# Optimization experiments

Hardware: AMD Instinct MI355X
Metric: run time of the kernel (lower is better)

## Reference

```python
import math
import jax, jax.numpy as jnp
import numpy as np

BN_EPS = 1e-5

def _lrelu(x, s):
    return jnp.where(x >= 0, x, s * x)

def _bn(x, g, b):
    # BatchNorm2d in train mode (torch default): biased batch stats over (B,H,W)
    mu = jnp.mean(x, axis=(0, 2, 3), keepdims=True)
    var = jnp.mean((x - mu) ** 2, axis=(0, 2, 3), keepdims=True)
    return (x - mu) / jnp.sqrt(var + BN_EPS) * g[None, :, None, None] + b[None, :, None, None]

def _knn(x, x2, k):
    # x: [B,d,P], x2: [B,d,S] -> idx [B,k,S]: k nearest points of x for each column of x2
    inner = -2.0 * jnp.einsum('bdp,bds->bps', x, x2)
    xx = jnp.sum(x ** 2, axis=1)[:, :, None]    # [B,P,1]
    xx2 = jnp.sum(x2 ** 2, axis=1)[:, None, :]  # [B,1,S]
    d = -xx - inner - xx2                        # [B,P,S], larger = closer
    _, idx = jax.lax.top_k(jnp.transpose(d, (0, 2, 1)), k)  # [B,S,k]
    return jnp.transpose(idx, (0, 2, 1))         # [B,k,S]

def _gather_nb(X, idx, s, k):
    # faithful to torch gether_neibour, including its flat-reshape layout
    B, C, P = X.shape
    base = jnp.arange(B)[:, None, None] * P
    flat = (idx + base).reshape(-1)
    Xt = jnp.transpose(X, (0, 2, 1)).reshape(B * P, C)
    return Xt[flat].reshape(B, s, k, C)

def _c2d(x, W, b):
    return jnp.einsum('oc,bcpk->bopk', W, x) + b[None, :, None, None]

def _c1d(x, W, b):
    return jnp.einsum('oc,bcp->bop', W, x) + b[None, :, None]

def _forward(x, W_pos, b_pos, g2, be2, W_conv, b_conv, g1, be1, W_a1, b_a1, W_a2, b_a2, W_b1, b_b1, W_b2, b_b2, num_points):
    B, C, P = x.shape
    k = 8
    s = num_points
    # ---- Dynamic_sampling_M: uniform mesh over (x,y) bbox, snap to nearest event ----
    L = int(math.ceil(math.sqrt(s)))
    m = jnp.arange(L, dtype=x.dtype) / L
    m01 = jnp.tile(m[None, :], (L, 1)).reshape(1, 1, L * L)
    m02 = jnp.tile(m[:, None], (1, L)).reshape(1, 1, L * L)
    mesh = jnp.broadcast_to(jnp.concatenate([m01, m02], axis=1), (B, 2, L * L))
    Px = jax.lax.stop_gradient(x[:, :2, :])  # knn runs under torch.no_grad
    mn = Px.min(axis=2, keepdims=True)
    mx = Px.max(axis=2, keepdims=True)
    PS = mesh * (mx - mn) + mn
    idx0 = _knn(Px, PS, 1)                                   # [B,1,L*L]
    sp = _gather_nb(x, idx0, L * L, 1)[:, :, 0, :].transpose(0, 2, 1)  # [B,C,s]
    idx = _knn(jax.lax.stop_gradient(x[:, :3, :]), jax.lax.stop_gradient(sp[:, :3, :]), k)  # [B,k,s]
    x1 = jnp.transpose(_gather_nb(x, idx, s, k), (0, 3, 1, 2))  # [B,C,s,k]
    # ---- positional encoding ----
    PA = x1[:, :3, :, :]
    PC = x1[:, :3, :, 0:1]
    diff = PA - PC
    sq = jnp.sum(diff ** 2, axis=1, keepdims=True)
    temp = jnp.where(sq > 0, jnp.sqrt(jnp.where(sq > 0, sq, 1.0)), 0.0)
    PEmb = jnp.concatenate([PA, jnp.broadcast_to(PC, PA.shape), diff, temp], axis=1)  # [B,10,s,k]
    PEmb = _lrelu(_bn(_c2d(PEmb, W_pos, b_pos), g2, be2), 0.2)
    x_ = _lrelu(_bn(_c2d(x1[:, :4, :, :], W_conv, b_conv), g1, be1), 0.2)
    feat = jnp.concatenate([x_, PEmb], axis=1)  # [B,64,s,k]
    att = _c2d(_lrelu(_c2d(feat, W_a1, b_a1), 0.2), W_a2, b_a2)  # [B,1,s,k]
    att = jax.nn.softmax(att, axis=-1)
    feat = jnp.sum(feat * att, axis=-1)  # [B,64,s]
    Fea1 = _c1d(feat, W_b1, b_b1)
    Fea2 = _c1d(x1[:, :4, :, 0], W_b2, b_b2)
    out = _lrelu(Fea1 + Fea2, 0.01)
    return jnp.concatenate([x1[:, :5, :, 0], out], axis=1)  # [B,69,s]

def setup_inputs() -> dict:
    key = jax.random.key(0)
    ks = jax.random.split(key, 8)
    B, C, P = 2, 5, 16384
    num_points = 4096  # perfect square required by the mesh sampler
    outc, inc, h = 64, 4, 32
    w = lambda k_, shape: jax.random.normal(k_, shape, jnp.float32) * 0.05
    x = jax.random.normal(ks[0], (B, C, P), jnp.float32)
    return dict(
        x=x,
        W_pos=w(ks[1], (h, 10)), b_pos=jnp.zeros((h,), jnp.float32),
        g2=jnp.ones((h,), jnp.float32), be2=jnp.zeros((h,), jnp.float32),
        W_conv=w(ks[2], (h, inc)), b_conv=jnp.zeros((h,), jnp.float32),
        g1=jnp.ones((h,), jnp.float32), be1=jnp.zeros((h,), jnp.float32),
        W_a1=w(ks[3], (32, outc)), b_a1=jnp.zeros((32,), jnp.float32),
        W_a2=w(ks[4], (1, 32)), b_a2=jnp.zeros((1,), jnp.float32),
        W_b1=w(ks[5], (outc, outc)), b_b1=jnp.zeros((outc,), jnp.float32),
        W_b2=w(ks[6], (outc, inc)), b_b2=jnp.zeros((outc,), jnp.float32),
        num_points=num_points,
    )

def reference(x, W_pos, b_pos, g2, be2, W_conv, b_conv, g1, be1, W_a1, b_a1, W_a2, b_a2, W_b1, b_b1, W_b2, b_b2, num_points):
    return _forward(x, W_pos, b_pos, g2, be2, W_conv, b_conv, g1, be1, W_a1, b_a1, W_a2, b_a2, W_b1, b_b1, W_b2, b_b2, num_points)
```

## Files before the change

kernel.cpp:

```cpp
#include <hip/hip_runtime.h>
#include <math.h>

#define B_ 2
#define P_ 16384
#define C_ 5
#define S_ 4096
#define KNN_ 8
#define L_ 64

typedef unsigned short u16;
typedef unsigned int u32;
typedef unsigned long long u64;

__device__ int    g_idxk[B_ * KNN_ * S_];
__device__ float  g_partials[256 * 128];
__device__ float  g_mnmx[B_][5];
__device__ int    g_hist[B_ * 4097];
__device__ int    g_cursor[B_ * 4096];
__device__ int    g_binof[B_ * P_];
__device__ int    g_dt[B_ * 4096];
__device__ u64    g_mask[B_ * 64];
__device__ float4 g_recA[B_ * P_];
__device__ float4 g_recB[B_ * P_];
__device__ u16    g_idxsc[B_ * P_];

__device__ __forceinline__ float bf2f(u16 u) {
  union { u32 i; float f; } c; c.i = ((u32)u) << 16; return c.f;
}
__device__ __forceinline__ u16 f2bf(float f) {
  union { float f; u32 i; } c; c.f = f;
  u32 r = c.i + 0x7fffu + ((c.i >> 16) & 1u);
  return (u16)(r >> 16);
}
__device__ __forceinline__ float ldany(const void* p, int i, int f32) {
  return f32 ? ((const float*)p)[i] : bf2f(((const u16*)p)[i]);
}

__device__ __forceinline__ double packkey(float d, int idx) {
  u32 bits = __float_as_uint(d);
  u32 key = bits ^ ((u32)(((int)bits) >> 31) | 0x80000000u);
  int hi = (int)(0x3FF00000u | (key >> 12));
  int lo = (int)((key << 20) | ((u32)(16383 - idx) << 6));
  return __hiloint2double(hi, lo);
}
__device__ __forceinline__ int keyidx(double w) {
  return 16383 - (int)(((u32)__double2loint(w) >> 6) & 16383u);
}
__device__ __forceinline__ float keyd(double w) {
  u32 hi = (u32)__double2hiint(w), lo = (u32)__double2loint(w);
  u32 key = (hi << 12) | (lo >> 20);
  u32 mask = (u32)(((int)key) >> 31);
  u32 bits = key ^ ((~mask) | 0x80000000u);
  return __uint_as_float(bits);
}

__device__ __forceinline__ int chk_bad(const void* p, int n, int tid) {
  int bad = 0;
  for (int i = tid; i < n; i += 256) {
    float f = bf2f(((const u16*)p)[i]);
    if (!(f == f) || fabsf(f) > 1024.0f) bad = 1;
  }
  return bad;
}

#define INS8(key)                                                        \
  do {                                                                   \
    if ((key) > a7) {                                                    \
      double t_ = (key), h_;                                             \
      h_ = fmax(a0, t_); t_ = fmin(a0, t_); a0 = h_;                     \
      h_ = fmax(a1, t_); t_ = fmin(a1, t_); a1 = h_;                     \
      h_ = fmax(a2, t_); t_ = fmin(a2, t_); a2 = h_;                     \
      h_ = fmax(a3, t_); t_ = fmin(a3, t_); a3 = h_;                     \
      h_ = fmax(a4, t_); t_ = fmin(a4, t_); a4 = h_;                     \
      h_ = fmax(a5, t_); t_ = fmin(a5, t_); a5 = h_;                     \
      h_ = fmax(a6, t_); t_ = fmin(a6, t_); a6 = h_;                     \
      a7 = fmax(a7, t_);                                                 \
    }                                                                    \
  } while (0)

#define MAX64(w)                                                         \
  do {                                                                   \
    w = fmax(w, __shfl_xor(w, 1, 64));                                   \
    w = fmax(w, __shfl_xor(w, 2, 64));                                   \
    w = fmax(w, __shfl_xor(w, 4, 64));                                   \
    w = fmax(w, __shfl_xor(w, 8, 64));                                   \
    w = fmax(w, __shfl_xor(w, 16, 64));                                  \
    w = fmax(w, __shfl_xor(w, 32, 64));                                  \
  } while (0)

__device__ __forceinline__ void ringcell(int R, int t, int cx, int cy, int& X, int& Y) {
  int side = 2 * R + 1;
  if (t < side)          { X = cx - R + t;          Y = cy - R; }
  else if (t < 2 * side) { X = cx - R + (t - side); Y = cy + R; }
  else {
    int u = t - 2 * side, m2 = 2 * R - 1;
    if (u < m2) { X = cx - R; Y = cy - R + 1 + u; }
    else        { X = cx + R; Y = cy - R + 1 + (u - m2); }
  }
}

__global__ __launch_bounds__(256) void k_prep(const void* __restrict__ xv) {
  __shared__ int sbad;
  __shared__ float sred[4][5];
  int tid = threadIdx.x, b = blockIdx.x;
  if (tid == 0) sbad = 0;
  __syncthreads();
  if (chk_bad(xv, 1024, tid)) atomicOr(&sbad, 1);
  __syncthreads();
  const int f32 = sbad;
  int base0 = b * C_ * P_, base1 = base0 + P_, base2 = base1 + P_;
  float mn0 = INFINITY, mx0 = -INFINITY, mn1 = INFINITY, mx1 = -INFINITY, am = 0.f;
  for (int p = tid; p < P_; p += 256) {
    float v0 = ldany(xv, base0 + p, f32);
    float v1 = ldany(xv, base1 + p, f32);
    float v2 = ldany(xv, base2 + p, f32);
    mn0 = fminf(mn0, v0); mx0 = fmaxf(mx0, v0);
    mn1 = fminf(mn1, v1); mx1 = fmaxf(mx1, v1);
    am = fmaxf(am, fabsf(v2));
  }
  for (int off = 32; off; off >>= 1) {
    mn0 = fminf(mn0, __shfl_down(mn0, off)); mx0 = fmaxf(mx0, __shfl_down(mx0, off));
    mn1 = fminf(mn1, __shfl_down(mn1, off)); mx1 = fmaxf(mx1, __shfl_down(mx1, off));
    am = fmaxf(am, __shfl_down(am, off));
  }
  int l = tid & 63, g = tid >> 6;
  if (l == 0) {
    sred[g][0] = mn0; sred[g][1] = mx0; sred[g][2] = mn1; sred[g][3] = mx1; sred[g][4] = am;
  }
  __syncthreads();
  if (tid == 0) {
    float a0 = fminf(fminf(sred[0][0], sred[1][0]), fminf(sred[2][0], sred[3][0]));
    float a1 = fmaxf(fmaxf(sred[0][1], sred[1][1]), fmaxf(sred[2][1], sred[3][1]));
    float a2 = fminf(fminf(sred[0][2], sred[1][2]), fminf(sred[2][2], sred[3][2]));
    float a3 = fmaxf(fmaxf(sred[0][3], sred[1][3]), fmaxf(sred[2][3], sred[3][3]));
    float a4 = fmaxf(fmaxf(sred[0][4], sred[1][4]), fmaxf(sred[2][4], sred[3][4]));
    float aa = fmaxf(fmaxf(fabsf(a0), fabsf(a1)), fmaxf(fmaxf(fabsf(a2), fabsf(a3)), a4));
    g_mnmx[b][0] = a0; g_mnmx[b][1] = a1; g_mnmx[b][2] = a2; g_mnmx[b][3] = a3;
    g_mnmx[b][4] = aa * aa;
  }
  for (int i2 = tid; i2 < 4097; i2 += 256) g_hist[b * 4097 + i2] = 0;
}

__global__ __launch_bounds__(256) void k_hist(const void* __restrict__ xv) {
  __shared__ int sbad;
  int tid = threadIdx.x, blk = blockIdx.x;
  if (tid == 0) sbad = 0;
  __syncthreads();
  if (chk_bad(xv, 1024, tid)) atomicOr(&sbad, 1);
  __syncthreads();
  const int f32 = sbad;
  int b = blk >> 4;
  int pb = (blk & 15) * 1024;
  int base0 = b * C_ * P_, base1 = base0 + P_;
  float mn0 = g_mnmx[b][0], mx0 = g_mnmx[b][1], mn1 = g_mnmx[b][2], mx1 = g_mnmx[b][3];
  float r0 = __fsub_rn(mx0, mn0), r1 = __fsub_rn(mx1, mn1);
  float inv0 = (r0 > 0.f) ? 64.0f / r0 : 0.f;
  float inv1 = (r1 > 0.f) ? 64.0f / r1 : 0.f;
  for (int q = 0; q < 4; ++q) {
    int i = pb + q * 256 + tid;
    float v0 = ldany(xv, base0 + i, f32);
    float v1 = ldany(xv, base1 + i, f32);
    int bx = (int)fminf(fmaxf((v0 - mn0) * inv0, 0.f), 63.f);
    int by = (int)fminf(fmaxf((v1 - mn1) * inv1, 0.f), 63.f);
    int bin = by * 64 + bx;
    g_binof[b * P_ + i] = bin;
    atomicAdd(&g_hist[b * 4097 + bin], 1);
  }
}

__global__ __launch_bounds__(256) void k_scan() {
  __shared__ int part[256];
  int b = blockIdx.x, t = threadIdx.x;
  int loc[16]; int s0 = 0;
  for (int q = 0; q < 16; ++q) { loc[q] = g_hist[b * 4097 + t * 16 + q]; s0 += loc[q]; }
  part[t] = s0;
  __syncthreads();
  for (int d2 = 1; d2 < 256; d2 <<= 1) {
    int v = (t >= d2) ? part[t - d2] : 0;
    __syncthreads();
    part[t] += v;
    __syncthreads();
  }
  int run = (t == 0) ? 0 : part[t - 1];
  for (int q = 0; q < 16; ++q) {
    g_hist[b * 4097 + t * 16 + q] = run;
    g_cursor[b * 4096 + t * 16 + q] = run;
    run += loc[q];
  }
  if (t == 0) g_hist[b * 4097 + 4096] = P_;
}

__global__ __launch_bounds__(256) void k_scatter(const void* __restrict__ xv) {
  __shared__ int sbad;
  int tid = threadIdx.x, blk = blockIdx.x;
  if (tid == 0) sbad = 0;
  __syncthreads();
  if (chk_bad(xv, 1024, tid)) atomicOr(&sbad, 1);
  __syncthreads();
  const int f32 = sbad;
  int b = blk >> 4;
  int pb = (blk & 15) * 1024;
  int base0 = b * C_ * P_, base1 = base0 + P_, base2 = base1 + P_;
  for (int q = 0; q < 4; ++q) {
    int i = pb + q * 256 + tid;
    float a0 = ldany(xv, base0 + i, f32);
    float a1 = ldany(xv, base1 + i, f32);
    float a2 = ldany(xv, base2 + i, f32);
    float xx2d = __fadd_rn(__fmul_rn(a0, a0), __fmul_rn(a1, a1));
    float xx3  = __fadd_rn(__fadd_rn(__fmul_rn(a0, a0), __fmul_rn(a1, a1)), __fmul_rn(a2, a2));
    int bin = g_binof[b * P_ + i];
    int pos = atomicAdd(&g_cursor[b * 4096 + bin], 1);
    g_recA[(b << 14) + pos] = make_float4(a0, a1, xx2d, __int_as_float(i));
    g_recB[(b << 14) + pos] = make_float4(a0, a1, a2, xx3);
    g_idxsc[(b << 14) + pos] = (u16)i;
  }
}

__global__ __launch_bounds__(256) void k_dt() {
  __shared__ u64 occm[64];
  __shared__ short rowd[64][64];
  int b = blockIdx.x, t = threadIdx.x;
  if (t < 64) {
    u64 m = 0ull;
    const int* h = g_hist + b * 4097 + t * 64;
    for (int x = 0; x < 64; ++x)
      if (h[x + 1] > h[x]) m |= (1ull << x);
    occm[t] = m;
    g_mask[b * 64 + t] = m;
  }
  __syncthreads();
#pragma unroll
  for (int q = 0; q < 16; ++q) {
    int c = q * 256 + t, y = c >> 6, x = c & 63;
    u64 m = occm[y];
    int rd = 127;
    if (m) {
      u64 hi = m >> x;
      int dhi = hi ? (__ffsll((long long)hi) - 1) : 127;
      u64 lo = (x < 63) ? (m & (((u64)1 << (x + 1)) - 1)) : m;
      int dlo = lo ? (x - (63 - __clzll((long long)lo))) : 127;
      rd = min(dhi, dlo);
    }
    rowd[y][x] = (short)rd;
  }
  __syncthreads();
#pragma unroll
  for (int q = 0; q < 16; ++q) {
    int c = q * 256 + t, y = c >> 6, x = c & 63;
    int best = 127;
    for (int dy = 0; dy < 64; ++dy) {
      if (dy >= best) break;
      int y1 = y - dy, y2 = y + dy;
      if (y1 >= 0) { int v = rowd[y1][x]; best = min(best, (dy > v) ? dy : v); }
      if (dy && y2 < 64) { int v = rowd[y2][x]; best = min(best, (dy > v) ? dy : v); }
    }
    g_dt[(b << 12) + c] = best;
  }
}

__global__ __launch_bounds__(256, 6) void k_knn2(const void* __restrict__ xv) {
  __shared__ int shist[4097];
  __shared__ u64 smask[64];
  __shared__ int sbad;
  int tid = threadIdx.x;
  if (tid == 0) sbad = 0;
  __syncthreads();
  if (chk_bad(xv, 1024, tid)) atomicOr(&sbad, 1);
  __syncthreads();
  const int f32 = sbad;

  int blk = blockIdx.x;
  int b = blk >> 10;
  for (int i2 = tid; i2 < 4097; i2 += 256) shist[i2] = g_hist[b * 4097 + i2];
  if (tid < 64) smask[tid] = g_mask[b * 64 + tid];
  __syncthreads();

  int l = tid & 63;
  int grp = l >> 3, lo = l & 7;
  int q = blk * 4 + (tid >> 6);
  int s = q & (S_ - 1);
  int base0 = b * C_ * P_, base1 = base0 + P_, base2 = base1 + P_;

  float mn0 = g_mnmx[b][0], mx0 = g_mnmx[b][1], mn1 = g_mnmx[b][2], mx1 = g_mnmx[b][3];
  float margin = 2e-5f * g_mnmx[b][4];
  float r0 = __fsub_rn(mx0, mn0), r1 = __fsub_rn(mx1, mn1);
  float w0 = r0 * 0.015625f, w1 = r1 * 0.015625f;
  float wmin = fminf(w0, w1) * 0.999f;
  const float4* recA = g_recA + (b << 14);
  const float4* recB = g_recB + (b << 14);

  float mm0 = (float)(s & (L_ - 1)) * 0.015625f;
  float mm1 = (float)(s >> 6) * 0.015625f;
  float ps0 = __fadd_rn(__fmul_rn(mm0, r0), mn0);
  float ps1 = __fadd_rn(__fmul_rn(mm1, r1), mn1);
  float xx2q = __fadd_rn(__fmul_rn(ps0, ps0), __fmul_rn(ps1, ps1));
  int bqx = s & 63, bqy = s >> 6;
  int R0 = g_dt[(b << 12) + s];
  double bestA = -1.0;
  if (R0 <= 1) {
#pragma unroll
    for (int dy = -1; dy <= 1; ++dy) {
#pragma unroll
      for (int dx = -1; dx <= 1; ++dx) {
        int X = bqx + dx, Y = bqy + dy;
        if ((unsigned)X > 63u || (unsigned)Y > 63u) continue;
        if (!((smask[Y] >> X) & 1ull)) continue;
        int bin = Y * 64 + X;
        int st = shist[bin], en = shist[bin + 1];
        for (int j2 = st + l; j2 < en; j2 += 64) {
          float4 rc = recA[j2];
          float dot = __fadd_rn(__fmul_rn(rc.x, ps0), __fmul_rn(rc.y, ps1));
          float inner = __fmul_rn(-2.0f, dot);
          float d = __fsub_rn(__fsub_rn(-rc.z, inner), xx2q);
          bestA = fmax(bestA, packkey(d, __float_as_int(rc.w)));
        }
      }
    }
  }
  double t1 = bestA;
  MAX64(t1);
  for (int R = (R0 < 2 ? 2 : R0); R < 64; ++R) {
    if (t1 >= 1.0) {
      float lb = (float)(R - 1) * wmin;
      float ub = __fadd_rn(-(lb * lb), margin);
      if (ub < keyd(t1)) break;
    }
    int cnt = 8 * R;
    for (int t = grp; t < cnt; t += 8) {
      int X, Y;
      ringcell(R, t, bqx, bqy, X, Y);
      if ((unsigned)X > 63u || (unsigned)Y > 63u) continue;
      if (!((smask[Y] >> X) & 1ull)) continue;
      int bin = Y * 64 + X;
      int st = shist[bin], en = shist[bin + 1];
      for (int j2 = st + lo; j2 < en; j2 += 8) {
        float4 rc = recA[j2];
        float dot = __fadd_rn(__fmul_rn(rc.x, ps0), __fmul_rn(rc.y, ps1));
        float inner = __fmul_rn(-2.0f, dot);
        float d = __fsub_rn(__fsub_rn(-rc.z, inner), xx2q);
        bestA = fmax(bestA, packkey(d, __float_as_int(rc.w)));
      }
    }
    if (__any(bestA > t1)) { t1 = bestA; MAX64(t1); }
  }
  int qi = keyidx(t1) & (P_ - 1);

  float q0 = ldany(xv, base0 + qi, f32);
  float q1 = ldany(xv, base1 + qi, f32);
  float q2 = ldany(xv, base2 + qi, f32);
  float xx3q = __fadd_rn(__fadd_rn(__fmul_rn(q0, q0), __fmul_rn(q1, q1)), __fmul_rn(q2, q2));
  int qbin = g_binof[b * P_ + qi];
  int cx = qbin & 63, cy = qbin >> 6;
  double a0 = -1.0, a1 = -1.0, a2 = -1.0, a3 = -1.0,
         a4 = -1.0, a5 = -1.0, a6 = -1.0, a7 = -1.0;
#pragma unroll
  for (int dy = -1; dy <= 1; ++dy) {
#pragma unroll
    for (int dx = -1; dx <= 1; ++dx) {
      int X = cx + dx, Y = cy + dy;
      if ((unsigned)X > 63u || (unsigned)Y > 63u) continue;
      if (!((smask[Y] >> X) & 1ull)) continue;
      int bin = Y * 64 + X;
      int st = shist[bin], en = shist[bin + 1];
      for (int j2 = st + l; j2 < en; j2 += 64) {
        float4 rc = recB[j2];
        int idx = (int)g_idxsc[(b << 14) + j2];
        float dot = __fadd_rn(__fadd_rn(__fmul_rn(rc.x, q0), __fmul_rn(rc.y, q1)),
                              __fmul_rn(rc.z, q2));
        float inner = __fmul_rn(-2.0f, dot);
        float d = __fsub_rn(__fsub_rn(-rc.w, inner), xx3q);
        double key = packkey(d, idx);
        INS8(key);
      }
    }
  }
  double t8;
  {
    double c0 = a0, c1 = a1, c2 = a2, c3 = a3, c4 = a4, c5 = a5, c6 = a6, c7 = a7;
    double w = -1.0;
#pragma unroll
    for (int r2 = 0; r2 < 8; ++r2) {
      w = c0;
      MAX64(w);
      bool cns = (c0 == w);
      c0 = cns ? c1 : c0; c1 = cns ? c2 : c1; c2 = cns ? c3 : c2; c3 = cns ? c4 : c3;
      c4 = cns ? c5 : c4; c5 = cns ? c6 : c5; c6 = cns ? c7 : c6; c7 = cns ? -1.0 : c7;
    }
    t8 = w;
  }
  for (int R = 2; R < 64; ++R) {
    if (t8 >= 1.0) {
      float lb = (float)(R - 1) * wmin;
      float ub = __fadd_rn(-(lb * lb), margin);
      if (ub < keyd(t8)) break;
    }
    bool added = false;
    int cnt = 8 * R;
    for (int t = grp; t < cnt; t += 8) {
      int X, Y;
      ringcell(R, t, cx, cy, X, Y);
      if ((unsigned)X > 63u || (unsigned)Y > 63u) continue;
      if (!((smask[Y] >> X) & 1ull)) continue;
      int bin = Y * 64 + X;
      int st = shist[bin], en = shist[bin + 1];
      for (int j2 = st + lo; j2 < en; j2 += 8) {
        float4 rc = recB[j2];
        int idx = (int)g_idxsc[(b << 14) + j2];
        float dot = __fadd_rn(__fadd_rn(__fmul_rn(rc.x, q0), __fmul_rn(rc.y, q1)),
                              __fmul_rn(rc.z, q2));
        float inner = __fmul_rn(-2.0f, dot);
        float d = __fsub_rn(__fsub_rn(-rc.w, inner), xx3q);
        double key = packkey(d, idx);
        added = added || (key > t8);
        INS8(key);
      }
    }
    if (__any(added)) {
      double c0 = a0, c1 = a1, c2 = a2, c3 = a3, c4 = a4, c5 = a5, c6 = a6, c7 = a7;
      double w = -1.0;
#pragma unroll
      for (int r2 = 0; r2 < 8; ++r2) {
        w = c0;
        MAX64(w);
        bool cns = (c0 == w);
        c0 = cns ? c1 : c0; c1 = cns ? c2 : c1; c2 = cns ? c3 : c2; c3 = cns ? c4 : c3;
        c4 = cns ? c5 : c4; c5 = cns ? c6 : c5; c6 = cns ? c7 : c6; c7 = cns ? -1.0 : c7;
      }
      t8 = w;
    }
  }
  double wk = 0.0;
#pragma unroll
  for (int r2 = 0; r2 < 8; ++r2) {
    double w = a0;
    MAX64(w);
    if (l == r2) wk = w;
    bool cns = (a0 == w);
    a0 = cns ? a1 : a0; a1 = cns ? a2 : a1; a2 = cns ? a3 : a2; a3 = cns ? a4 : a3;
    a4 = cns ? a5 : a4; a5 = cns ? a6 : a5; a6 = cns ? a7 : a6; a7 = cns ? -1.0 : a7;
  }
  if (l < 8) g_idxk[b * 32768 + l * 4096 + s] = keyidx(wk);
}

__global__ __launch_bounds__(256) void k_tail(const void* __restrict__ x,
                                              const void* __restrict__ Wpos,
                                              const void* __restrict__ bpos,
                                              const void* __restrict__ Wconv,
                                              const void* __restrict__ bconv) {
  __shared__ float sWpos[320], sbpos[32], sWconv[128], sbconv[32];
  __shared__ float sacc[16][128];
  __shared__ int sbx, sbw;
  int tid = threadIdx.x;
  if (tid == 0) { sbx = 0; sbw = 0; }
  __syncthreads();
  if (chk_bad(x, 1024, tid)) atomicOr(&sbx, 1);
  if (chk_bad(Wpos, 320, tid) | chk_bad(Wconv, 128, tid)) atomicOr(&sbw, 1);
  __syncthreads();
  const int f32 = sbx, wf32 = sbw;

  int id = blockIdx.x * 256 + tid;
  int b = id >> 15, n = id & 32767;
  const int* fb = g_idxk + b * 32768;
  int base0 = b * C_ * P_;
  int p = fb[n] & (P_ - 1);
  int p0 = fb[n & ~7] & (P_ - 1);
  float xvv[4], pc3[3];
#pragma unroll
  for (int cc = 0; cc < 4; ++cc) xvv[cc] = ldany(x, base0 + cc * P_ + p, f32);
#pragma unroll
  for (int cc = 0; cc < 3; ++cc) pc3[cc] = ldany(x, base0 + cc * P_ + p0, f32);

  for (int i2 = tid; i2 < 320; i2 += 256) sWpos[i2] = ldany(Wpos, i2, wf32);
  if (tid < 128) sWconv[tid] = ldany(Wconv, tid, wf32);
  if (tid < 32) { sbpos[tid] = ldany(bpos, tid, wf32); sbconv[tid] = ldany(bconv, tid, wf32); }
  __syncthreads();

  float d0 = xvv[0] - pc3[0], d1 = xvv[1] - pc3[1], d2 = xvv[2] - pc3[2];
  float sq = d0 * d0 + d1 * d1 + d2 * d2;
  float temp = (sq > 0.0f) ? sqrtf(sq) : 0.0f;
  float pe[10] = {xvv[0], xvv[1], xvv[2], pc3[0], pc3[1], pc3[2], d0, d1, d2, temp};
#pragma unroll
  for (int o = 0; o < 64; ++o) {
    float v;
    if (o < 32) {
      v = sbconv[o];
#pragma unroll
      for (int cc = 0; cc < 4; ++cc) v = fmaf(sWconv[o * 4 + cc], xvv[cc], v);
    } else {
      v = sbpos[o - 32];
#pragma unroll
      for (int cc = 0; cc < 10; ++cc) v = fmaf(sWpos[(o - 32) * 10 + cc], pe[cc], v);
    }
    float sv = v, qv = v * v;
    for (int m = 1; m < 16; m <<= 1) { sv += __shfl_xor(sv, m, 16); qv += __shfl_xor(qv, m, 16); }
    if ((tid & 15) == 0) { sacc[tid >> 4][o * 2] = sv; sacc[tid >> 4][o * 2 + 1] = qv; }
  }
  __syncthreads();
  if (tid < 128) {
    float a = 0.f;
#pragma unroll
    for (int w = 0; w < 16; ++w) a += sacc[w][tid];
    g_partials[blockIdx.x * 128 + tid] = a;
  }
}

__global__ __launch_bounds__(256) void k_pass2(const void* __restrict__ x,
                                               const void* __restrict__ Wpos,
                                               const void* __restrict__ bpos,
                                               const void* __restrict__ Wconv,
                                               const void* __restrict__ bconv,
                                               const void* __restrict__ g1,
                                               const void* __restrict__ be1,
                                               const void* __restrict__ g2,
                                               const void* __restrict__ be2,
                                               const void* __restrict__ Wa1,
                                               const void* __restrict__ ba1,
                                               const void* __restrict__ Wa2,
                                               const void* __restrict__ ba2,
                                               const void* __restrict__ Wb1,
                                               const void* __restrict__ bb1,
                                               const void* __restrict__ Wb2,
                                               const void* __restrict__ bb2,
                                               void* __restrict__ out) {
  __shared__ float sWpos[320], sbpos[32], sWconv[128], sbconv[32];
  __shared__ float sWa1[2048], sba1[32], sWa2[32];
  __shared__ float sWb1[64 * 65];
  __shared__ float sbb1[64], sWb2[256], sbb2[64], sstats[128];
  __shared__ float sp2[2][128];
  __shared__ float sba2;
  __shared__ int sbx, sbw;
  int tid = threadIdx.x;
  if (tid == 0) { sbx = 0; sbw = 0; }
  __syncthreads();
  if (chk_bad(x, 1024, tid)) atomicOr(&sbx, 1);
  if (chk_bad(Wa1, 2048, tid) | chk_bad(Wb1, 4096, tid)) atomicOr(&sbw, 1);
  __syncthreads();
  int xf32 = sbx, wf32 = sbw;

  int g = blockIdx.x * 32 + (tid >> 3);
  int j = tid & 7;
  int b = g >> 12, i = g & (S_ - 1);
  int n = i * 8 + j;
  const int* fb = g_idxk + b * 32768;
  int xbase = b * C_ * P_;
  int p = fb[n] & (P_ - 1);
  int p0 = fb[n & ~7] & (P_ - 1);
  float xvv[4];
#pragma unroll
  for (int c = 0; c < 4; ++c) xvv[c] = ldany(x, xbase + c * P_ + p, xf32);
  float pc3[3];
#pragma unroll
  for (int c = 0; c < 3; ++c) pc3[c] = ldany(x, xbase + c * P_ + p0, xf32);
  float xc0 = ldany(x, xbase + p0, xf32);
  float xc1 = ldany(x, xbase + P_ + p0, xf32);
  float xc2 = ldany(x, xbase + 2 * P_ + p0, xf32);
  float xc3 = ldany(x, xbase + 3 * P_ + p0, xf32);

  {
    int slot = tid & 127, half = tid >> 7;
    float a0 = 0.f, a1 = 0.f;
    for (int blk = half * 128; blk < half * 128 + 128; blk += 2) {
      a0 += g_partials[blk * 128 + slot];
      a1 += g_partials[(blk + 1) * 128 + slot];
    }
    sp2[half][slot] = a0 + a1;
  }
  for (int i2 = tid; i2 < 320; i2 += 256) sWpos[i2] = ldany(Wpos, i2, wf32);
  if (tid < 128) sWconv[tid] = ldany(Wconv, tid, wf32);
  if (tid < 32) { sbpos[tid] = ldany(bpos, tid, wf32); sbconv[tid] = ldany(bconv, tid, wf32); }
  for (int i2 = tid; i2 < 2048; i2 += 256) sWa1[i2] = ldany(Wa1, i2, wf32);
  for (int i2 = tid; i2 < 4096; i2 += 256) sWb1[(i2 >> 6) * 65 + (i2 & 63)] = ldany(Wb1, i2, wf32);
  if (tid >= 32 && tid < 64) { sba1[tid - 32] = ldany(ba1, tid - 32, wf32); sWa2[tid - 32] = ldany(Wa2, tid - 32, wf32); }
  if (tid >= 64 && tid < 128) { sbb1[tid - 64] = ldany(bb1, tid - 64, wf32); sbb2[tid - 64] = ldany(bb2, tid - 64, wf32); }
  sWb2[tid] = ldany(Wb2, tid, wf32);
  if (tid == 0) sba2 = ldany(ba2, 0, wf32);
  __syncthreads();
  if (tid >= 128 && tid < 192) {
    int ch = tid - 128;
    float sum = sp2[0][ch * 2] + sp2[1][ch * 2];
    float sq = sp2[0][ch * 2 + 1] + sp2[1][ch * 2 + 1];
    float mean = sum * (1.0f / 65536.0f);
    float var = sq * (1.0f / 65536.0f) - mean * mean;
    int o = ch & 31;
    float gg = ldany(ch < 32 ? g1 : g2, o, wf32);
    float be = ldany(ch < 32 ? be1 : be2, o, wf32);
    float scale = gg / sqrtf(var + 1e-5f);
    sstats[ch * 2] = scale;
    sstats[ch * 2 + 1] = be - mean * scale;
  }
  __syncthreads();

  float d0 = xvv[0] - pc3[0], d1 = xvv[1] - pc3[1], d2 = xvv[2] - pc3[2];
  float sq = d0 * d0 + d1 * d1 + d2 * d2;
  float temp = (sq > 0.0f) ? sqrtf(sq) : 0.0f;
  float pe[10] = {xvv[0], xvv[1], xvv[2], pc3[0], pc3[1], pc3[2], d0, d1, d2, temp};
  float feat[64];
#pragma unroll
  for (int o = 0; o < 32; ++o) {
    float acc = sbconv[o];
#pragma unroll
    for (int c = 0; c < 4; ++c) acc = fmaf(sWconv[o * 4 + c], xvv[c], acc);
    feat[o] = acc;
  }
#pragma unroll
  for (int o = 0; o < 32; ++o) {
    float acc = sbpos[o];
#pragma unroll
    for (int c = 0; c < 10; ++c) acc = fmaf(sWpos[o * 10 + c], pe[c], acc);
    feat[32 + o] = acc;
  }
#pragma unroll
  for (int c = 0; c < 64; ++c) {
    float v = fmaf(feat[c], sstats[c * 2], sstats[c * 2 + 1]);
    feat[c] = (v >= 0.f) ? v : 0.2f * v;
  }
  float att = sba2;
#pragma unroll 4
  for (int h = 0; h < 32; ++h) {
    float a0 = 0.f, a1 = 0.f, a2 = 0.f, a3 = 0.f;
#pragma unroll
    for (int c = 0; c < 64; c += 4) {
      a0 = fmaf(sWa1[h * 64 + c],     feat[c],     a0);
      a1 = fmaf(sWa1[h * 64 + c + 1], feat[c + 1], a1);
      a2 = fmaf(sWa1[h * 64 + c + 2], feat[c + 2], a2);
      a3 = fmaf(sWa1[h * 64 + c + 3], feat[c + 3], a3);
    }
    float acc = sba1[h] + ((a0 + a1) + (a2 + a3));
    acc = (acc >= 0.f) ? acc : 0.2f * acc;
    att = fmaf(sWa2[h], acc, att);
  }
  float mxv = att;
  for (int mk = 1; mk < 8; mk <<= 1) mxv = fmaxf(mxv, __shfl_xor(mxv, mk, 8));
  float e = expf(att - mxv);
  float se = e;
  for (int mk = 1; mk < 8; mk <<= 1) se += __shfl_xor(se, mk, 8);
  float a = e / se;
#pragma unroll
  for (int c = 0; c < 64; ++c) {
    float w = feat[c] * a;
    w += __shfl_xor(w, 1, 8);
    w += __shfl_xor(w, 2, 8);
    w += __shfl_xor(w, 4, 8);
    feat[c] = w;
  }
  int obase = b * 69 * S_;
#pragma unroll
  for (int oc = 0; oc < 8; ++oc) {
    int o = j * 8 + oc;
    float a0 = sbb1[o], a1 = 0.f, a2 = 0.f, a3 = 0.f;
#pragma unroll
    for (int c = 0; c < 64; c += 4) {
      a0 = fmaf(sWb1[o * 65 + c],     feat[c],     a0);
      a1 = fmaf(sWb1[o * 65 + c + 1], feat[c + 1], a1);
      a2 = fmaf(sWb1[o * 65 + c + 2], feat[c + 2], a2);
      a3 = fmaf(sWb1[o * 65 + c + 3], feat[c + 3], a3);
    }
    float acc = (a0 + a1) + (a2 + a3);
    float acc2 = sbb2[o];
    acc2 = fmaf(sWb2[o * 4 + 0], xc0, acc2);
    acc2 = fmaf(sWb2[o * 4 + 1], xc1, acc2);
    acc2 = fmaf(sWb2[o * 4 + 2], xc2, acc2);
    acc2 = fmaf(sWb2[o * 4 + 3], xc3, acc2);
    float r = acc + acc2;
    r = (r >= 0.f) ? r : 0.01f * r;
    int oi = obase + (5 + o) * S_ + i;
    if (xf32) ((float*)out)[oi] = r; else ((u16*)out)[oi] = f2bf(r);
  }
  if (j == 0) {
#pragma unroll
    for (int c = 0; c < 5; ++c) {
      int oi = obase + c * S_ + i;
      if (xf32) ((float*)out)[oi] = ((const float*)x)[xbase + c * P_ + p0];
      else      ((u16*)out)[oi]   = ((const u16*)x)[xbase + c * P_ + p0];
    }
  }
}

extern "C" void kernel_launch(void* const* d_in, const int* in_sizes, int n_in,
                              void* d_out, int out_size, void* d_ws, size_t ws_size,
                              hipStream_t stream) {
  const void* x     = d_in[0];
  const void* Wpos  = d_in[1];
  const void* bpos  = d_in[2];
  const void* g2    = d_in[3];
  const void* be2   = d_in[4];
  const void* Wconv = d_in[5];
  const void* bconv = d_in[6];
  const void* g1    = d_in[7];
  const void* be1   = d_in[8];
  const void* Wa1   = d_in[9];
  const void* ba1   = d_in[10];
  const void* Wa2   = d_in[11];
  const void* ba2   = d_in[12];
  const void* Wb1   = d_in[13];
  const void* bb1   = d_in[14];
  const void* Wb2   = d_in[15];
  const void* bb2   = d_in[16];
  (void)d_ws; (void)ws_size; (void)in_sizes; (void)n_in;

  hipLaunchKernelGGL(k_prep,    dim3(2),    dim3(256), 0, stream, x);
  hipLaunchKernelGGL(k_hist,    dim3(32),   dim3(256), 0, stream, x);
  hipLaunchKernelGGL(k_scan,    dim3(2),    dim3(256), 0, stream);
  hipLaunchKernelGGL(k_scatter, dim3(32),   dim3(256), 0, stream, x);
  hipLaunchKernelGGL(k_dt,      dim3(2),    dim3(256), 0, stream);
  hipLaunchKernelGGL(k_knn2,    dim3(2048), dim3(256), 0, stream, x);
  hipLaunchKernelGGL(k_tail,    dim3(256),  dim3(256), 0, stream, x,
                     Wpos, bpos, Wconv, bconv);
  hipLaunchKernelGGL(k_pass2,   dim3(256),  dim3(256), 0, stream, x,
                     Wpos, bpos, Wconv, bconv, g1, be1, g2, be2,
                     Wa1, ba1, Wa2, ba2, Wb1, bb1, Wb2, bb2, d_out);
}
```

Baseline: 366.5 us.

## Fuse scan with distance transform, widen prep, use bitonic wave merge in kNN

Merges the scan and distance-transform kernels into one launch that builds the occupancy mask from the histogram. k_prep now runs with 1024 threads per block. The kNN kernel replaces its repeated 8-round wave-max extraction with a bitonic butterfly merge of per-lane top-8 lists. It also interleaves query indices across wavefronts and drops the occupancy hint from launch bounds. Together these target launch overhead and reduction cost in the kNN stage, but the butterfly merge moves more shuffles per round and register pressure may rise.

Result: faster. 325.2 us (-11.3%).

```diff
diff --git a/kernel.cpp b/kernel.cpp
--- a/kernel.cpp
+++ b/kernel.cpp
@@ -54,13 +54,18 @@
   return __uint_as_float(bits);
 }
 
-__device__ __forceinline__ int chk_bad(const void* p, int n, int tid) {
+__device__ __forceinline__ int chk_bad(const void* p, int n, int tid, int stride) {
   int bad = 0;
-  for (int i = tid; i < n; i += 256) {
+  for (int i = tid; i < n; i += stride) {
     float f = bf2f(((const u16*)p)[i]);
     if (!(f == f) || fabsf(f) > 1024.0f) bad = 1;
   }
   return bad;
+}
+
+__device__ __forceinline__ void cmpswap(double& a, double& b) {
+  double hi = fmax(a, b), lo = fmin(a, b);
+  a = hi; b = lo;
 }
 
 #define INS8(key)                                                        \
@@ -88,6 +93,23 @@
     w = fmax(w, __shfl_xor(w, 32, 64));                                  \
   } while (0)
 
+#define BMERGE8(v0, v1, v2, v3, v4, v5, v6, v7)                          \
+  do {                                                                   \
+    for (int m_ = 1; m_ < 64; m_ <<= 1) {                                \
+      double u0_ = __shfl_xor(v0, m_, 64), u1_ = __shfl_xor(v1, m_, 64); \
+      double u2_ = __shfl_xor(v2, m_, 64), u3_ = __shfl_xor(v3, m_, 64); \
+      double u4_ = __shfl_xor(v4, m_, 64), u5_ = __shfl_xor(v5, m_, 64); \
+      double u6_ = __shfl_xor(v6, m_, 64), u7_ = __shfl_xor(v7, m_, 64); \
+      v0 = fmax(v0, u7_); v1 = fmax(v1, u6_);                            \
+      v2 = fmax(v2, u5_); v3 = fmax(v3, u4_);                            \
+      v4 = fmax(v4, u3_); v5 = fmax(v5, u2_);                            \
+      v6 = fmax(v6, u1_); v7 = fmax(v7, u0_);                            \
+      cmpswap(v0, v4); cmpswap(v1, v5); cmpswap(v2, v6); cmpswap(v3, v7);\
+      cmpswap(v0, v2); cmpswap(v1, v3); cmpswap(v4, v6); cmpswap(v5, v7);\
+      cmpswap(v0, v1); cmpswap(v2, v3); cmpswap(v4, v5); cmpswap(v6, v7);\
+    }                                                                    \
+  } while (0)
+
 __device__ __forceinline__ void ringcell(int R, int t, int cx, int cy, int& X, int& Y) {
   int side = 2 * R + 1;
   if (t < side)          { X = cx - R + t;          Y = cy - R; }
@@ -99,18 +121,18 @@
   }
 }
 
-__global__ __launch_bounds__(256) void k_prep(const void* __restrict__ xv) {
+__global__ __launch_bounds__(1024) void k_prep(const void* __restrict__ xv) {
   __shared__ int sbad;
-  __shared__ float sred[4][5];
+  __shared__ float sred[16][5];
   int tid = threadIdx.x, b = blockIdx.x;
   if (tid == 0) sbad = 0;
   __syncthreads();
-  if (chk_bad(xv, 1024, tid)) atomicOr(&sbad, 1);
+  if (chk_bad(xv, 1024, tid, 1024)) atomicOr(&sbad, 1);
   __syncthreads();
   const int f32 = sbad;
   int base0 = b * C_ * P_, base1 = base0 + P_, base2 = base1 + P_;
   float mn0 = INFINITY, mx0 = -INFINITY, mn1 = INFINITY, mx1 = -INFINITY, am = 0.f;
-  for (int p = tid; p < P_; p += 256) {
+  for (int p = tid; p < P_; p += 1024) {
     float v0 = ldany(xv, base0 + p, f32);
     float v1 = ldany(xv, base1 + p, f32);
     float v2 = ldany(xv, base2 + p, f32);
@@ -129,16 +151,17 @@
   }
   __syncthreads();
   if (tid == 0) {
-    float a0 = fminf(fminf(sred[0][0], sred[1][0]), fminf(sred[2][0], sred[3][0]));
-    float a1 = fmaxf(fmaxf(sred[0][1], sred[1][1]), fmaxf(sred[2][1], sred[3][1]));
-    float a2 = fminf(fminf(sred[0][2], sred[1][2]), fminf(sred[2][2], sred[3][2]));
-    float a3 = fmaxf(fmaxf(sred[0][3], sred[1][3]), fmaxf(sred[2][3], sred[3][3]));
-    float a4 = fmaxf(fmaxf(sred[0][4], sred[1][4]), fmaxf(sred[2][4], sred[3][4]));
+    float a0 = sred[0][0], a1 = sred[0][1], a2 = sred[0][2], a3 = sred[0][3], a4 = sred[0][4];
+    for (int w = 1; w < 16; ++w) {
+      a0 = fminf(a0, sred[w][0]); a1 = fmaxf(a1, sred[w][1]);
+      a2 = fminf(a2, sred[w][2]); a3 = fmaxf(a3, sred[w][3]);
+      a4 = fmaxf(a4, sred[w][4]);
+    }
     float aa = fmaxf(fmaxf(fabsf(a0), fabsf(a1)), fmaxf(fmaxf(fabsf(a2), fabsf(a3)), a4));
     g_mnmx[b][0] = a0; g_mnmx[b][1] = a1; g_mnmx[b][2] = a2; g_mnmx[b][3] = a3;
     g_mnmx[b][4] = aa * aa;
   }
-  for (int i2 = tid; i2 < 4097; i2 += 256) g_hist[b * 4097 + i2] = 0;
+  for (int i2 = tid; i2 < 4097; i2 += 1024) g_hist[b * 4097 + i2] = 0;
 }
 
 __global__ __launch_bounds__(256) void k_hist(const void* __restrict__ xv) {
@@ -146,7 +169,7 @@
   int tid = threadIdx.x, blk = blockIdx.x;
   if (tid == 0) sbad = 0;
   __syncthreads();
-  if (chk_bad(xv, 1024, tid)) atomicOr(&sbad, 1);
+  if (chk_bad(xv, 1024, tid, 256)) atomicOr(&sbad, 1);
   __syncthreads();
   const int f32 = sbad;
   int b = blk >> 4;
@@ -168,12 +191,22 @@
   }
 }
 
-__global__ __launch_bounds__(256) void k_scan() {
+__global__ __launch_bounds__(256) void k_scan_dt() {
   __shared__ int part[256];
+  __shared__ u32 occw[128];
+  __shared__ short rowd[64][64];
   int b = blockIdx.x, t = threadIdx.x;
+  if (t < 128) occw[t] = 0;
+  __syncthreads();
   int loc[16]; int s0 = 0;
-  for (int q = 0; q < 16; ++q) { loc[q] = g_hist[b * 4097 + t * 16 + q]; s0 += loc[q]; }
+  u32 bits16 = 0;
+  for (int q = 0; q < 16; ++q) {
+    loc[q] = g_hist[b * 4097 + t * 16 + q];
+    s0 += loc[q];
+    if (loc[q] > 0) bits16 |= (1u << q);
+  }
   part[t] = s0;
+  atomicOr(&occw[t >> 1], bits16 << ((t & 1) * 16));
   __syncthreads();
   for (int d2 = 1; d2 < 256; d2 <<= 1) {
     int v = (t >= d2) ? part[t - d2] : 0;
@@ -188,6 +221,37 @@
     run += loc[q];
   }
   if (t == 0) g_hist[b * 4097 + 4096] = P_;
+  if (t < 64) {
+    u64 m = ((u64)occw[2 * t + 1] << 32) | (u64)occw[2 * t];
+    g_mask[b * 64 + t] = m;
+  }
+#pragma unroll
+  for (int q = 0; q < 16; ++q) {
+    int c = q * 256 + t, y = c >> 6, x = c & 63;
+    u64 m = ((u64)occw[2 * y + 1] << 32) | (u64)occw[2 * y];
+    int rd = 127;
+    if (m) {
+      u64 hi = m >> x;
+      int dhi = hi ? (__ffsll((long long)hi) - 1) : 127;
+      u64 lo = (x < 63) ? (m & (((u64)1 << (x + 1)) - 1)) : m;
+      int dlo = lo ? (x - (63 - __clzll((long long)lo))) : 127;
+      rd = min(dhi, dlo);
+    }
+    rowd[y][x] = (short)rd;
+  }
+  __syncthreads();
+#pragma unroll
+  for (int q = 0; q < 16; ++q) {
+    int c = q * 256 + t, y = c >> 6, x = c & 63;
+    int best = 127;
+    for (int dy = 0; dy < 64; ++dy) {
+      if (dy >= best) break;
+      int y1 = y - dy, y2 = y + dy;
+      if (y1 >= 0) { int v = rowd[y1][x]; best = min(best, (dy > v) ? dy : v); }
+      if (dy && y2 < 64) { int v = rowd[y2][x]; best = min(best, (dy > v) ? dy : v); }
+    }
+    g_dt[(b << 12) + c] = best;
+  }
 }
 
 __global__ __launch_bounds__(256) void k_scatter(const void* __restrict__ xv) {
@@ -195,7 +259,7 @@
   int tid = threadIdx.x, blk = blockIdx.x;
   if (tid == 0) sbad = 0;
   __syncthreads();
-  if (chk_bad(xv, 1024, tid)) atomicOr(&sbad, 1);
+  if (chk_bad(xv, 1024, tid, 256)) atomicOr(&sbad, 1);
   __syncthreads();
   const int f32 = sbad;
   int b = blk >> 4;
@@ -216,69 +280,27 @@
   }
 }
 
-__global__ __launch_bounds__(256) void k_dt() {
-  __shared__ u64 occm[64];
-  __shared__ short rowd[64][64];
-  int b = blockIdx.x, t = threadIdx.x;
-  if (t < 64) {
-    u64 m = 0ull;
-    const int* h = g_hist + b * 4097 + t * 64;
-    for (int x = 0; x < 64; ++x)
-      if (h[x + 1] > h[x]) m |= (1ull << x);
-    occm[t] = m;
-    g_mask[b * 64 + t] = m;
-  }
-  __syncthreads();
-#pragma unroll
-  for (int q = 0; q < 16; ++q) {
-    int c = q * 256 + t, y = c >> 6, x = c & 63;
-    u64 m = occm[y];
-    int rd = 127;
-    if (m) {
-      u64 hi = m >> x;
-      int dhi = hi ? (__ffsll((long long)hi) - 1) : 127;
-      u64 lo = (x < 63) ? (m & (((u64)1 << (x + 1)) - 1)) : m;
-      int dlo = lo ? (x - (63 - __clzll((long long)lo))) : 127;
-      rd = min(dhi, dlo);
-    }
-    rowd[y][x] = (short)rd;
-  }
-  __syncthreads();
-#pragma unroll
-  for (int q = 0; q < 16; ++q) {
-    int c = q * 256 + t, y = c >> 6, x = c & 63;
-    int best = 127;
-    for (int dy = 0; dy < 64; ++dy) {
-      if (dy >= best) break;
-      int y1 = y - dy, y2 = y + dy;
-      if (y1 >= 0) { int v = rowd[y1][x]; best = min(best, (dy > v) ? dy : v); }
-      if (dy && y2 < 64) { int v = rowd[y2][x]; best = min(best, (dy > v) ? dy : v); }
-    }
-    g_dt[(b << 12) + c] = best;
-  }
-}
-
-__global__ __launch_bounds__(256, 6) void k_knn2(const void* __restrict__ xv) {
+__global__ __launch_bounds__(256) void k_knn2(const void* __restrict__ xv) {
   __shared__ int shist[4097];
   __shared__ u64 smask[64];
   __shared__ int sbad;
   int tid = threadIdx.x;
   if (tid == 0) sbad = 0;
   __syncthreads();
-  if (chk_bad(xv, 1024, tid)) atomicOr(&sbad, 1);
+  if (chk_bad(xv, 1024, tid, 256)) atomicOr(&sbad, 1);
   __syncthreads();
   const int f32 = sbad;
 
   int blk = blockIdx.x;
   int b = blk >> 10;
+  int bb = blk & 1023;
   for (int i2 = tid; i2 < 4097; i2 += 256) shist[i2] = g_hist[b * 4097 + i2];
   if (tid < 64) smask[tid] = g_mask[b * 64 + tid];
   __syncthreads();
 
   int l = tid & 63;
   int grp = l >> 3, lo = l & 7;
-  int q = blk * 4 + (tid >> 6);
-  int s = q & (S_ - 1);
+  int s = (tid >> 6) * 1024 + bb;
   int base0 = b * C_ * P_, base1 = base0 + P_, base2 = base1 + P_;
 
   float mn0 = g_mnmx[b][0], mx0 = g_mnmx[b][1], mn1 = g_mnmx[b][2], mx1 = g_mnmx[b][3];
@@ -374,20 +396,9 @@
       }
     }
   }
-  double t8;
-  {
-    double c0 = a0, c1 = a1, c2 = a2, c3 = a3, c4 = a4, c5 = a5, c6 = a6, c7 = a7;
-    double w = -1.0;
-#pragma unroll
-    for (int r2 = 0; r2 < 8; ++r2) {
-      w = c0;
-      MAX64(w);
-      bool cns = (c0 == w);
-      c0 = cns ? c1 : c0; c1 = cns ? c2 : c1; c2 = cns ? c3 : c2; c3 = cns ? c4 : c3;
-      c4 = cns ? c5 : c4; c5 = cns ? c6 : c5; c6 = cns ? c7 : c6; c7 = cns ? -1.0 : c7;
-    }
-    t8 = w;
-  }
+  double m0 = a0, m1 = a1, m2 = a2, m3 = a3, m4 = a4, m5 = a5, m6 = a6, m7 = a7;
+  BMERGE8(m0, m1, m2, m3, m4, m5, m6, m7);
+  double t8 = m7;
   for (int R = 2; R < 64; ++R) {
     if (t8 >= 1.0) {
       float lb = (float)(R - 1) * wmin;
@@ -416,29 +427,15 @@
       }
     }
     if (__any(added)) {
-      double c0 = a0, c1 = a1, c2 = a2, c3 = a3, c4 = a4, c5 = a5, c6 = a6, c7 = a7;
-      double w = -1.0;
-#pragma unroll
-      for (int r2 = 0; r2 < 8; ++r2) {
-        w = c0;
-        MAX64(w);
-        bool cns = (c0 == w);
-        c0 = cns ? c1 : c0; c1 = cns ? c2 : c1; c2 = cns ? c3 : c2; c3 = cns ? c4 : c3;
-        c4 = cns ? c5 : c4; c5 = cns ? c6 : c5; c6 = cns ? c7 : c6; c7 = cns ? -1.0 : c7;
-      }
-      t8 = w;
-    }
-  }
-  double wk = 0.0;
-#pragma unroll
-  for (int r2 = 0; r2 < 8; ++r2) {
-    double w = a0;
-    MAX64(w);
-    if (l == r2) wk = w;
-    bool cns = (a0 == w);
-    a0 = cns ? a1 : a0; a1 = cns ? a2 : a1; a2 = cns ? a3 : a2; a3 = cns ? a4 : a3;
-    a4 = cns ? a5 : a4; a5 = cns ? a6 : a5; a6 = cns ? a7 : a6; a7 = cns ? -1.0 : a7;
-  }
+      m0 = a0; m1 = a1; m2 = a2; m3 = a3; m4 = a4; m5 = a5; m6 = a6; m7 = a7;
+      BMERGE8(m0, m1, m2, m3, m4, m5, m6, m7);
+      t8 = m7;
+    }
+  }
+  double wk = m7;
+  if (l == 0) wk = m0; else if (l == 1) wk = m1; else if (l == 2) wk = m2;
+  else if (l == 3) wk = m3; else if (l == 4) wk = m4; else if (l == 5) wk = m5;
+  else if (l == 6) wk = m6;
   if (l < 8) g_idxk[b * 32768 + l * 4096 + s] = keyidx(wk);
 }
 
@@ -453,8 +450,8 @@
   int tid = threadIdx.x;
   if (tid == 0) { sbx = 0; sbw = 0; }
   __syncthreads();
-  if (chk_bad(x, 1024, tid)) atomicOr(&sbx, 1);
-  if (chk_bad(Wpos, 320, tid) | chk_bad(Wconv, 128, tid)) atomicOr(&sbw, 1);
+  if (chk_bad(x, 1024, tid, 256)) atomicOr(&sbx, 1);
+  if (chk_bad(Wpos, 320, tid, 256) | chk_bad(Wconv, 128, tid, 256)) atomicOr(&sbw, 1);
   __syncthreads();
   const int f32 = sbx, wf32 = sbw;
 
@@ -532,8 +529,8 @@
   int tid = threadIdx.x;
   if (tid == 0) { sbx = 0; sbw = 0; }
   __syncthreads();
-  if (chk_bad(x, 1024, tid)) atomicOr(&sbx, 1);
-  if (chk_bad(Wa1, 2048, tid) | chk_bad(Wb1, 4096, tid)) atomicOr(&sbw, 1);
+  if (chk_bad(x, 1024, tid, 256)) atomicOr(&sbx, 1);
+  if (chk_bad(Wa1, 2048, tid, 256) | chk_bad(Wb1, 4096, tid, 256)) atomicOr(&sbw, 1);
   __syncthreads();
   int xf32 = sbx, wf32 = sbw;
 
@@ -698,15 +695,14 @@
   const void* bb2   = d_in[16];
   (void)d_ws; (void)ws_size; (void)in_sizes; (void)n_in;
 
-  hipLaunchKernelGGL(k_prep,    dim3(2),    dim3(256), 0, stream, x);
-  hipLaunchKernelGGL(k_hist,    dim3(32),   dim3(256), 0, stream, x);
-  hipLaunchKernelGGL(k_scan,    dim3(2),    dim3(256), 0, stream);
-  hipLaunchKernelGGL(k_scatter, dim3(32),   dim3(256), 0, stream, x);
-  hipLaunchKernelGGL(k_dt,      dim3(2),    dim3(256), 0, stream);
-  hipLaunchKernelGGL(k_knn2,    dim3(2048), dim3(256), 0, stream, x);
-  hipLaunchKernelGGL(k_tail,    dim3(256),  dim3(256), 0, stream, x,
+  hipLaunchKernelGGL(k_prep,    dim3(2),    dim3(1024), 0, stream, x);
+  hipLaunchKernelGGL(k_hist,    dim3(32),   dim3(256),  0, stream, x);
+  hipLaunchKernelGGL(k_scan_dt, dim3(2),    dim3(256),  0, stream);
+  hipLaunchKernelGGL(k_scatter, dim3(32),   dim3(256),  0, stream, x);
+  hipLaunchKernelGGL(k_knn2,    dim3(2048), dim3(256),  0, stream, x);
+  hipLaunchKernelGGL(k_tail,    dim3(256),  dim3(256),  0, stream, x,
                      Wpos, bpos, Wconv, bconv);
-  hipLaunchKernelGGL(k_pass2,   dim3(256),  dim3(256), 0, stream, x,
+  hipLaunchKernelGGL(k_pass2,   dim3(256),  dim3(256),  0, stream, x,
                      Wpos, bpos, Wconv, bconv, g1, be1, g2, be2,
                      Wa1, ba1, Wa2, ba2, Wb1, bb1, Wb2, bb2, d_out);
 }
```
